# Kernel optimization log

Hardware: AMD Instinct MI355X
Metric: run time of the kernel (lower is better)

## Reference

```python
import jax, jax.numpy as jnp
import numpy as np

ROPE_DIM = 64       # config.rope_dim
GN_GROUPS = 32      # config.group_norm_num
GN_CHANNELS = 2048  # config.group_norm_channels == intermediate_size
GN_EPS = 1e-5


def rope_rotate(x):
    """lucidrains rotary-embedding-torch rotate_queries_or_keys:
    interleaved-pair rotation of the first ROPE_DIM features, rest pass through."""
    T = x.shape[-2]
    inv_freq = 1.0 / (10000.0 ** (jnp.arange(0, ROPE_DIM, 2, dtype=jnp.float32) / ROPE_DIM))
    freqs = jnp.arange(T, dtype=jnp.float32)[:, None] * inv_freq[None, :]  # (T, ROPE_DIM/2)
    freqs = jnp.repeat(freqs, 2, axis=-1)                                  # (T, ROPE_DIM)
    cos, sin = jnp.cos(freqs), jnp.sin(freqs)
    xr = x[..., :ROPE_DIM]
    x1, x2 = xr[..., 0::2], xr[..., 1::2]
    rot = jnp.stack((-x2, x1), axis=-1).reshape(xr.shape)  # rotate_half, interleaved
    xr = xr * cos + rot * sin
    return jnp.concatenate([xr, x[..., ROPE_DIM:]], axis=-1)


def group_norm_rows(x2d, weight, bias):
    """torch GroupNorm on a 2D (N, C) input: normalize each group of channels per row."""
    N, Cc = x2d.shape
    xg = x2d.reshape(N, GN_GROUPS, Cc // GN_GROUPS)
    mu = xg.mean(-1, keepdims=True)
    var = xg.var(-1, keepdims=True)
    xn = ((xg - mu) * jax.lax.rsqrt(var + GN_EPS)).reshape(N, Cc)
    return xn * weight + bias


def setup_inputs() -> dict:
    key = jax.random.key(0)
    ks = jax.random.split(key, 4)
    B, T, I, C = 2, 4096, 2048, 2048
    X = jax.random.normal(ks[0], (B, T, I), dtype=jnp.float32)
    S_n = jnp.zeros((B, C), dtype=jnp.float32)
    W_Q = jax.random.normal(ks[1], (I, C), dtype=jnp.float32) / I
    hh_b = jax.random.normal(ks[2], (C,), dtype=jnp.float32) * 0.02  # nn.Linear bias of self.hh
    gn_weight = jnp.ones((C,), dtype=jnp.float32)
    gn_bias = jnp.zeros((C,), dtype=jnp.float32)
    return {"X": X, "S_n": S_n, "W_Q": W_Q, "hh_b": hh_b,
            "gn_weight": gn_weight, "gn_bias": gn_bias}


def reference(X, S_n, W_Q, hh_b, gn_weight, gn_bias):
    # forward_auto_rec with chunk_len = T (single chunk, h_t starts at zeros):
    #   Q = ReLU(rope(X @ W_Q));  H = tanh(hh(0) + Q) = tanh(Q + b_hh)
    # K, V and the decay-masked A = (H K^T * D) V are computed in the source but
    # discarded (out = H), so they are dead code (DCE'd under jit) and omitted.
    B, T, _ = X.shape
    Q = jax.nn.relu(rope_rotate(X @ W_Q))   # (B, T, C)
    H = jnp.tanh(Q + hh_b)                  # (B, T, C)
    C = H.shape[-1]
    # dropout in eval mode = identity
    out = group_norm_rows(H.reshape(-1, C), gn_weight, gn_bias).reshape(B, T, C)
    # out.transpose(-2,-1).contiguous().view(B,T,C): reshape of the transposed layout
    out = jnp.swapaxes(out, -2, -1).reshape(B, T, C)
    return out, S_n
```

## Files before the change

kernel.cpp:

```cpp
#include <hip/hip_runtime.h>

#define T_DIM 4096
#define C_DIM 2048
#define K_DIM 2048

typedef __bf16 bf16x8 __attribute__((ext_vector_type(8)));
typedef float f32x4 __attribute__((ext_vector_type(4)));

__device__ __forceinline__ unsigned short f2bf(float f) {
  union { float f; unsigned int i; } x;
  x.f = f;
  unsigned int r = x.i + 0x7fffu + ((x.i >> 16) & 1u);
  return (unsigned short)(r >> 16);
}

#define GLD16(gsrc, ldst)                                                   \
  __builtin_amdgcn_global_load_lds(                                         \
      (const __attribute__((address_space(1))) unsigned int*)(gsrc),        \
      (__attribute__((address_space(3))) unsigned int*)(ldst), 16, 0, 0)

__global__ __launch_bounds__(256) void transpose_w(const float* __restrict__ W,
                                                   unsigned short* __restrict__ Wt) {
  __shared__ float tile[64][68];
  const int c0 = blockIdx.x * 64;
  const int r0 = blockIdx.y * 64;
  const int tid = threadIdx.x;
#pragma unroll
  for (int i = 0; i < 4; ++i) {
    int s = tid + i * 256;
    int r = s >> 4, c4 = (s & 15) * 4;
    *(float4*)&tile[r][c4] = *(const float4*)&W[(size_t)(r0 + r) * C_DIM + c0 + c4];
  }
  __syncthreads();
#pragma unroll
  for (int i = 0; i < 2; ++i) {
    int s = tid + i * 256;
    int n = s >> 3, k8 = (s & 7) * 8;
    __align__(16) unsigned short tmp[8];
#pragma unroll
    for (int j = 0; j < 8; ++j) tmp[j] = f2bf(tile[k8 + j][n]);
    *(uint4*)&Wt[(size_t)(c0 + n) * K_DIM + r0 + k8] = *(uint4*)tmp;
  }
}

__global__ __launch_bounds__(256) void cvt_x(const float* __restrict__ X,
                                             unsigned short* __restrict__ Xb) {
  size_t base = (size_t)blockIdx.x * 2048 + (size_t)threadIdx.x * 8;
  float4 a = *(const float4*)&X[base];
  float4 b = *(const float4*)&X[base + 4];
  __align__(16) unsigned short t[8];
  t[0] = f2bf(a.x); t[1] = f2bf(a.y); t[2] = f2bf(a.z); t[3] = f2bf(a.w);
  t[4] = f2bf(b.x); t[5] = f2bf(b.y); t[6] = f2bf(b.z); t[7] = f2bf(b.w);
  *(uint4*)&Xb[base] = *(const uint4*)t;
}

#define FOR_MN(OP) \
  OP(0,0) OP(0,1) OP(0,2) OP(0,3) \
  OP(1,0) OP(1,1) OP(1,2) OP(1,3) \
  OP(2,0) OP(2,1) OP(2,2) OP(2,3) \
  OP(3,0) OP(3,1) OP(3,2) OP(3,3)

#define DECL_ACC(m,n) f32x4 a##m##n = {0.f, 0.f, 0.f, 0.f};

template <bool ABF16>
__global__ __launch_bounds__(256, 3) void gemm_fused(const void* __restrict__ Av,
                                                     const unsigned short* __restrict__ Wt,
                                                     const float* __restrict__ hhb,
                                                     const float* __restrict__ gnw,
                                                     const float* __restrict__ gnb,
                                                     float* __restrict__ out) {
  constexpr int SMEM_BYTES = ABF16 ? 34816 : 49152;
  __shared__ __align__(16) char smem[SMEM_BYTES];
  unsigned short* lsA = (unsigned short*)smem;
  float* lsAf = (float*)smem;
  unsigned short* lsB = (unsigned short*)(smem + (ABF16 ? 16384 : 32768));
  float(*lsO)[68] = (float(*)[68])smem;

  const int tid = threadIdx.x;
  const int wave = tid >> 6;
  const int lane = tid & 63;
  const int quad = lane >> 4;
  const int l16 = lane & 15;
  const int wm = wave >> 1, wn = wave & 1;

  const int bid = blockIdx.x;
  const int wg = (bid & 7) * 128 + (bid >> 3);
  const int m0 = (wg >> 4) * 128;
  const int n0 = (wg & 15) * 128;

  FOR_MN(DECL_ACC)

  const int srow = lane >> 3;
  const int scol = ((lane & 7) * 8) ^ ((srow & 7) << 3);
  const unsigned short* gA16 =
      ABF16 ? (const unsigned short*)Av + (size_t)(m0 + wave * 32 + srow) * K_DIM + scol
            : (const unsigned short*)0;
  const float* gA32 = ABF16 ? (const float*)0
                            : (const float*)Av + (size_t)(m0 + wave * 32 + (lane >> 4)) * K_DIM +
                                  (lane & 15) * 4;
  const unsigned short* gB = Wt + (size_t)(n0 + wave * 32 + srow) * K_DIM + scol;

  for (int k0 = 0; k0 < K_DIM; k0 += 64) {
    __syncthreads();
    if constexpr (ABF16) {
#pragma unroll
      for (int r = 0; r < 4; ++r) {
        GLD16(gA16 + (size_t)(r * 8) * K_DIM + k0, lsA + wave * 2048 + r * 512);
        GLD16(gB + (size_t)(r * 8) * K_DIM + k0, lsB + wave * 2048 + r * 512);
      }
    } else {
#pragma unroll
      for (int r = 0; r < 8; ++r)
        GLD16(gA32 + (size_t)(r * 4) * K_DIM + k0, lsAf + wave * 2048 + r * 256);
#pragma unroll
      for (int r = 0; r < 4; ++r)
        GLD16(gB + (size_t)(r * 8) * K_DIM + k0, lsB + wave * 2048 + r * 512);
    }
    __syncthreads();

#pragma unroll
    for (int kk = 0; kk < 2; ++kk) {
      const int xs = (kk * 32 + quad * 8) ^ ((l16 & 7) << 3);

#define LOAD_AF(m)                                                                   \
      bf16x8 af##m;                                                                  \
      if constexpr (ABF16) {                                                         \
        af##m = *(const bf16x8*)(const void*)(lsA + (wm * 64 + m * 16 + l16) * 64 + xs); \
      } else {                                                                       \
        const float* ap_ = lsAf + (wm * 64 + m * 16 + l16) * 64 + kk * 32 + quad * 8; \
        f32x4 a0_ = *(const f32x4*)ap_;                                              \
        f32x4 a1_ = *(const f32x4*)(ap_ + 4);                                        \
        af##m[0] = (__bf16)a0_[0]; af##m[1] = (__bf16)a0_[1];                        \
        af##m[2] = (__bf16)a0_[2]; af##m[3] = (__bf16)a0_[3];                        \
        af##m[4] = (__bf16)a1_[0]; af##m[5] = (__bf16)a1_[1];                        \
        af##m[6] = (__bf16)a1_[2]; af##m[7] = (__bf16)a1_[3];                        \
      }
#define LOAD_BF(n)                                                                   \
      bf16x8 bfr##n = *(const bf16x8*)(const void*)(lsB + (wn * 64 + n * 16 + l16) * 64 + xs);

      LOAD_AF(0) LOAD_AF(1) LOAD_AF(2) LOAD_AF(3)
      LOAD_BF(0) LOAD_BF(1) LOAD_BF(2) LOAD_BF(3)

#define MFMA_OP(m,n) \
      a##m##n = __builtin_amdgcn_mfma_f32_16x16x32_bf16(af##m, bfr##n, a##m##n, 0, 0, 0);
      FOR_MN(MFMA_OP)
#undef LOAD_AF
#undef LOAD_BF
    }
  }
  __syncthreads();

  const int c_base = n0 + wn * 64;
  const int t_base = (m0 & (T_DIM - 1)) + wm * 64;

#define LOADC(n)                                  \
  const int c##n = c_base + n * 16 + l16;         \
  const float hb##n = hhb[c##n];                  \
  const float gw##n = gnw[c##n];                  \
  const float gb##n = gnb[c##n];
  LOADC(0) LOADC(1) LOADC(2) LOADC(3)

  if (c_base == 0) {
#define ROPE_E(n,m,r)                                                   \
    { float v_ = a##m##n[r];                                            \
      float p_ = __shfl_xor(v_, 1, 64);                                 \
      int t_ = t_base + m * 16 + quad * 4 + r;                          \
      float ang_ = (float)t_ * fr_;                                     \
      float s_ = sinf(ang_);                                            \
      float co_ = cosf(ang_);                                           \
      a##m##n[r] = v_ * co_ + sg_ * p_ * s_; }
#define ROPE_M(n,m) ROPE_E(n,m,0) ROPE_E(n,m,1) ROPE_E(n,m,2) ROPE_E(n,m,3)
#define ROPE_N(n)                                                       \
    { int cc_ = n * 16 + l16;                                           \
      int ii_ = cc_ >> 1;                                               \
      float fr_ = expf(-(float)ii_ * 0.28782313662425572f);             \
      float sg_ = (cc_ & 1) ? 1.f : -1.f;                               \
      ROPE_M(n,0) ROPE_M(n,1) ROPE_M(n,2) ROPE_M(n,3) }
    ROPE_N(0) ROPE_N(1) ROPE_N(2) ROPE_N(3)
  }

#define GN_ROW(m,r)                                                     \
  { float h0_ = tanhf(fmaxf(a##m##0[r], 0.f) + hb0);                    \
    float h1_ = tanhf(fmaxf(a##m##1[r], 0.f) + hb1);                    \
    float h2_ = tanhf(fmaxf(a##m##2[r], 0.f) + hb2);                    \
    float h3_ = tanhf(fmaxf(a##m##3[r], 0.f) + hb3);                    \
    float s1_ = h0_ + h1_ + h2_ + h3_;                                  \
    float s2_ = h0_ * h0_ + h1_ * h1_ + h2_ * h2_ + h3_ * h3_;          \
    s1_ += __shfl_xor(s1_, 1, 64);  s2_ += __shfl_xor(s2_, 1, 64);      \
    s1_ += __shfl_xor(s1_, 2, 64);  s2_ += __shfl_xor(s2_, 2, 64);      \
    s1_ += __shfl_xor(s1_, 4, 64);  s2_ += __shfl_xor(s2_, 4, 64);      \
    s1_ += __shfl_xor(s1_, 8, 64);  s2_ += __shfl_xor(s2_, 8, 64);      \
    float mu_ = s1_ * 0.015625f;                                        \
    float var_ = s2_ * 0.015625f - mu_ * mu_;                           \
    float rs_ = rsqrtf(var_ + 1e-5f);                                   \
    a##m##0[r] = (h0_ - mu_) * rs_ * gw0 + gb0;                         \
    a##m##1[r] = (h1_ - mu_) * rs_ * gw1 + gb1;                         \
    a##m##2[r] = (h2_ - mu_) * rs_ * gw2 + gb2;                         \
    a##m##3[r] = (h3_ - mu_) * rs_ * gw3 + gb3; }
#define GN_M(m) GN_ROW(m,0) GN_ROW(m,1) GN_ROW(m,2) GN_ROW(m,3)
  GN_M(0) GN_M(1) GN_M(2) GN_M(3)

  const int bb = m0 >> 12;
  const int t0 = m0 & (T_DIM - 1);
#define ST_MN(m,n)                                                      \
  lsO[wn * 64 + n * 16 + l16][m * 16 + quad * 4 + 0] = a##m##n[0];      \
  lsO[wn * 64 + n * 16 + l16][m * 16 + quad * 4 + 1] = a##m##n[1];      \
  lsO[wn * 64 + n * 16 + l16][m * 16 + quad * 4 + 2] = a##m##n[2];      \
  lsO[wn * 64 + n * 16 + l16][m * 16 + quad * 4 + 3] = a##m##n[3];
#pragma unroll
  for (int h = 0; h < 2; ++h) {
    if (wm == h) {
      FOR_MN(ST_MN)
    }
    __syncthreads();
#pragma unroll
    for (int i = 0; i < 8; ++i) {
      int s = tid + i * 256;
      int cl = s >> 4;
      int t4 = (s & 15) * 4;
      float4 v = *(const float4*)&lsO[cl][t4];
      *(float4*)&out[(size_t)bb * C_DIM * T_DIM + (size_t)(n0 + cl) * T_DIM + t0 + h * 64 + t4] = v;
    }
    __syncthreads();
  }
}

__global__ __launch_bounds__(256) void copy_sn(const float* __restrict__ src,
                                               float* __restrict__ dst) {
  int i = blockIdx.x * 256 + threadIdx.x;
  dst[i] = src[i];
}

extern "C" void kernel_launch(void* const* d_in, const int* in_sizes, int n_in,
                              void* d_out, int out_size, void* d_ws, size_t ws_size,
                              hipStream_t stream) {
  const float* X = (const float*)d_in[0];
  const float* Sn = (const float*)d_in[1];
  const float* W = (const float*)d_in[2];
  const float* hhb = (const float*)d_in[3];
  const float* gnw = (const float*)d_in[4];
  const float* gnb = (const float*)d_in[5];
  float* out = (float*)d_out;

  unsigned short* Wt = (unsigned short*)d_ws;
  const size_t wt_bytes = (size_t)C_DIM * K_DIM * 2;
  const size_t xb_bytes = (size_t)2 * T_DIM * K_DIM * 2;

  transpose_w<<<dim3(32, 32), dim3(256), 0, stream>>>(W, Wt);

  if (ws_size >= wt_bytes + xb_bytes) {
    unsigned short* Xb = Wt + (size_t)C_DIM * K_DIM;
    cvt_x<<<dim3(8192), dim3(256), 0, stream>>>(X, Xb);
    gemm_fused<true><<<dim3(1024), dim3(256), 0, stream>>>(Xb, Wt, hhb, gnw, gnb, out);
  } else {
    gemm_fused<false><<<dim3(1024), dim3(256), 0, stream>>>(X, Wt, hhb, gnw, gnb, out);
  }

  copy_sn<<<dim3(16), dim3(256), 0, stream>>>(Sn, out + (size_t)16777216);
}
```

Baseline: 344.7 us.

## Double-buffer GEMM K-loop with async LDS loads and smaller K tile

Replaces the single-buffered 64-wide K loop with a double-buffered 32-wide K loop. The next tile is prefetched via global_load_lds while the current tile feeds the MFMAs, with explicit vmcnt waits and barriers, so load latency is meant to overlap compute. The LDS swizzle is reworked for the narrower rows. The cost is twice as many iterations and barriers per K step, and correctness now depends on the hand-written waitcnt values.

```diff
diff --git a/kernel.cpp b/kernel.cpp
--- a/kernel.cpp
+++ b/kernel.cpp
@@ -90,65 +90,92 @@
 
   FOR_MN(DECL_ACC)
 
-  const int srow = lane >> 3;
-  const int scol = ((lane & 7) * 8) ^ ((srow & 7) << 3);
+  const int srow16 = lane >> 2;
+  const int scol16 = (((lane & 3) ^ (srow16 & 3)) * 8);
+  const int srow32 = lane >> 3;
+  const int scol32 = (((lane & 7) ^ srow32) * 4);
+
   const unsigned short* gA16 =
-      ABF16 ? (const unsigned short*)Av + (size_t)(m0 + wave * 32 + srow) * K_DIM + scol
+      ABF16 ? (const unsigned short*)Av + (size_t)(m0 + wave * 32 + srow16) * K_DIM + scol16
             : (const unsigned short*)0;
-  const float* gA32 = ABF16 ? (const float*)0
-                            : (const float*)Av + (size_t)(m0 + wave * 32 + (lane >> 4)) * K_DIM +
-                                  (lane & 15) * 4;
-  const unsigned short* gB = Wt + (size_t)(n0 + wave * 32 + srow) * K_DIM + scol;
-
-  for (int k0 = 0; k0 < K_DIM; k0 += 64) {
-    __syncthreads();
+  const float* gA32 =
+      ABF16 ? (const float*)0
+            : (const float*)Av + (size_t)(m0 + wave * 32 + srow32) * K_DIM + scol32;
+  const unsigned short* gB16 =
+      Wt + (size_t)(n0 + wave * 32 + srow16) * K_DIM + scol16;
+
+  const int axs = (quad ^ (l16 & 3)) * 8;
+  const int abase = (wm * 64 + l16) * 32 + axs;
+  const int bbase = (wn * 64 + l16) * 32 + axs;
+  const int abasef = (wm * 64 + l16) * 32;
+  const int u0 = ((2 * quad) ^ (l16 & 7)) * 4;
+  const int u1 = ((2 * quad + 1) ^ (l16 & 7)) * 4;
+
+  auto stage = [&](int d, int koff) {
     if constexpr (ABF16) {
-#pragma unroll
-      for (int r = 0; r < 4; ++r) {
-        GLD16(gA16 + (size_t)(r * 8) * K_DIM + k0, lsA + wave * 2048 + r * 512);
-        GLD16(gB + (size_t)(r * 8) * K_DIM + k0, lsB + wave * 2048 + r * 512);
-      }
+      GLD16(gA16 + koff, lsA + d * 4096 + wave * 1024);
+      GLD16(gA16 + koff + 16 * K_DIM, lsA + d * 4096 + wave * 1024 + 512);
     } else {
-#pragma unroll
-      for (int r = 0; r < 8; ++r)
-        GLD16(gA32 + (size_t)(r * 4) * K_DIM + k0, lsAf + wave * 2048 + r * 256);
-#pragma unroll
-      for (int r = 0; r < 4; ++r)
-        GLD16(gB + (size_t)(r * 8) * K_DIM + k0, lsB + wave * 2048 + r * 512);
-    }
-    __syncthreads();
-
-#pragma unroll
-    for (int kk = 0; kk < 2; ++kk) {
-      const int xs = (kk * 32 + quad * 8) ^ ((l16 & 7) << 3);
-
-#define LOAD_AF(m)                                                                   \
-      bf16x8 af##m;                                                                  \
-      if constexpr (ABF16) {                                                         \
-        af##m = *(const bf16x8*)(const void*)(lsA + (wm * 64 + m * 16 + l16) * 64 + xs); \
-      } else {                                                                       \
-        const float* ap_ = lsAf + (wm * 64 + m * 16 + l16) * 64 + kk * 32 + quad * 8; \
-        f32x4 a0_ = *(const f32x4*)ap_;                                              \
-        f32x4 a1_ = *(const f32x4*)(ap_ + 4);                                        \
-        af##m[0] = (__bf16)a0_[0]; af##m[1] = (__bf16)a0_[1];                        \
-        af##m[2] = (__bf16)a0_[2]; af##m[3] = (__bf16)a0_[3];                        \
-        af##m[4] = (__bf16)a1_[0]; af##m[5] = (__bf16)a1_[1];                        \
-        af##m[6] = (__bf16)a1_[2]; af##m[7] = (__bf16)a1_[3];                        \
-      }
-#define LOAD_BF(n)                                                                   \
-      bf16x8 bfr##n = *(const bf16x8*)(const void*)(lsB + (wn * 64 + n * 16 + l16) * 64 + xs);
-
-      LOAD_AF(0) LOAD_AF(1) LOAD_AF(2) LOAD_AF(3)
-      LOAD_BF(0) LOAD_BF(1) LOAD_BF(2) LOAD_BF(3)
+      GLD16(gA32 + koff, lsAf + d * 4096 + wave * 1024);
+      GLD16(gA32 + koff + 8 * K_DIM, lsAf + d * 4096 + wave * 1024 + 256);
+      GLD16(gA32 + koff + 16 * K_DIM, lsAf + d * 4096 + wave * 1024 + 512);
+      GLD16(gA32 + koff + 24 * K_DIM, lsAf + d * 4096 + wave * 1024 + 768);
+    }
+    GLD16(gB16 + koff, lsB + d * 4096 + wave * 1024);
+    GLD16(gB16 + koff + 16 * K_DIM, lsB + d * 4096 + wave * 1024 + 512);
+  };
+
+  constexpr int NT = K_DIM / 32;
+
+  stage(0, 0);
+  for (int t = 0; t < NT; ++t) {
+    const int cur = t & 1;
+    if (t + 1 < NT) {
+      stage(cur ^ 1, (t + 1) * 32);
+      if constexpr (ABF16)
+        asm volatile("s_waitcnt vmcnt(4)" ::: "memory");
+      else
+        asm volatile("s_waitcnt vmcnt(6)" ::: "memory");
+    } else {
+      asm volatile("s_waitcnt vmcnt(0)" ::: "memory");
+    }
+    __builtin_amdgcn_s_barrier();
+    asm volatile("" ::: "memory");
+
+    const unsigned short* pa = lsA + cur * 4096;
+    const float* paf = lsAf + cur * 4096;
+    const unsigned short* pb = lsB + cur * 4096;
+
+#define LOAD_AF(m)                                                        \
+    bf16x8 af##m;                                                         \
+    if constexpr (ABF16) {                                                \
+      af##m = *(const bf16x8*)(const void*)(pa + abase + m * 512);        \
+    } else {                                                              \
+      const float* ap_ = paf + abasef + m * 512;                          \
+      f32x4 a0_ = *(const f32x4*)(ap_ + u0);                              \
+      f32x4 a1_ = *(const f32x4*)(ap_ + u1);                              \
+      af##m[0] = (__bf16)a0_[0]; af##m[1] = (__bf16)a0_[1];               \
+      af##m[2] = (__bf16)a0_[2]; af##m[3] = (__bf16)a0_[3];               \
+      af##m[4] = (__bf16)a1_[0]; af##m[5] = (__bf16)a1_[1];               \
+      af##m[6] = (__bf16)a1_[2]; af##m[7] = (__bf16)a1_[3];               \
+    }
+#define LOAD_BF(n)                                                        \
+    bf16x8 bfr##n = *(const bf16x8*)(const void*)(pb + bbase + n * 512);
+
+    LOAD_AF(0) LOAD_AF(1) LOAD_AF(2) LOAD_AF(3)
+    LOAD_BF(0) LOAD_BF(1) LOAD_BF(2) LOAD_BF(3)
 
 #define MFMA_OP(m,n) \
-      a##m##n = __builtin_amdgcn_mfma_f32_16x16x32_bf16(af##m, bfr##n, a##m##n, 0, 0, 0);
-      FOR_MN(MFMA_OP)
+    a##m##n = __builtin_amdgcn_mfma_f32_16x16x32_bf16(af##m, bfr##n, a##m##n, 0, 0, 0);
+    FOR_MN(MFMA_OP)
 #undef LOAD_AF
 #undef LOAD_BF
-    }
-  }
-  __syncthreads();
+
+    asm volatile("s_waitcnt lgkmcnt(0)" ::: "memory");
+    __builtin_amdgcn_sched_barrier(0);
+    __builtin_amdgcn_s_barrier();
+    asm volatile("" ::: "memory");
+  }
 
   const int c_base = n0 + wn * 64;
   const int t_base = (m0 & (T_DIM - 1)) + wm * 64;
```

Measured after the change: 342.6 us. No clear change (-0.6%).
